# Performance work log

Hardware: AMD Instinct MI355X
Metric: run time of the kernel (lower is better)

The kernel has to match this reference:

```python
import jax, jax.numpy as jnp
import numpy as np

T = 4096
C = 2048
N_FEAT = 2048
NEG = -1e30  # finite stand-in for -inf so fully-masked (padding) rows stay NaN-free


def setup_inputs() -> dict:
    key = jax.random.key(0)
    kx, kw, kb = jax.random.split(key, 3)
    x = jax.random.normal(kx, (T, C), dtype=jnp.float32)
    # Dense(features=3*n_feat): kernel (C, 3*n_feat), bias (3*n_feat,)
    W = jax.random.normal(kw, (C, 3 * N_FEAT), dtype=jnp.float32) * (1.0 / np.sqrt(C))
    b = jax.random.normal(kb, (3 * N_FEAT,), dtype=jnp.float32) * 0.01
    n_padd = 128
    return {"x": x, "W": W, "b": b, "n_padd": n_padd}


def reference(x, W, b, n_padd):
    T_, _ = x.shape
    qkv = x @ W + b                      # (T, 3*n_feat)
    q, k, v = jnp.split(qkv, 3, axis=1)  # each (T, n_feat)
    scale = 1.0 / jnp.sqrt(jnp.float32(q.shape[1]))
    att = (q @ k.T) * scale              # (T, T)
    rows = jnp.arange(T_)[:, None]
    cols = jnp.arange(T_)[None, :]
    # causal AND both row/col past the left padding
    mask = (cols <= rows) & (cols >= n_padd) & (rows >= n_padd)
    att = jnp.where(mask, att, NEG)
    p = jax.nn.softmax(att, axis=1)      # stable row softmax
    # kernel only stores rows >= n_padd; padding rows are zero
    p = jnp.where(rows >= n_padd, p, 0.0)
    y = p @ v                            # (T, n_feat)
    return y
```

## Files before the change

### kernel.cpp

```cpp
#include <hip/hip_runtime.h>
#include <cstdint>


#define T_DIM 4096
#define C_DIM 2048
#define NF    2048
#define N3    6144
#define NEGV  (-1e30f)

typedef __bf16 bf16x8 __attribute__((ext_vector_type(8)));
typedef __bf16 bf16x4 __attribute__((ext_vector_type(4)));
typedef float  f32x4  __attribute__((ext_vector_type(4)));

#define FENCE() asm volatile("" ::: "memory")
#define BARRIER() do { FENCE(); __builtin_amdgcn_s_barrier(); FENCE(); } while (0)

__device__ __forceinline__ void async_cp16(const void* g, void* l) {
    __builtin_amdgcn_global_load_lds(
        reinterpret_cast<const __attribute__((address_space(1))) unsigned int*>(
            reinterpret_cast<uintptr_t>(g)),
        reinterpret_cast<__attribute__((address_space(3))) unsigned int*>(
            reinterpret_cast<uintptr_t>(l)),
        16, 0, 0);
}

__device__ __forceinline__ void gemm256(const __bf16* A, const __bf16* B,
                                        int lda, int ldb, int m0, int n0,
                                        int kiters, __bf16* As, __bf16* Bs,
                                        f32x4 (&acc)[8][4]) {
    if (kiters <= 0) return;
    const int t    = threadIdx.x;
    const int wv   = t >> 6;
    const int lane = t & 63;
    const int srow = t >> 3;
    const int scol = (((t & 7) ^ (srow & 7)) << 3);
    const int wmo  = (wv >> 2) * 128;
    const int wno  = (wv & 3) * 64;
    const int lrow = lane & 15;
    const int kq   = lane >> 4;
    const int swz  = lrow & 7;
    const int rc0  = ((kq ^ swz) << 3);
    const int rc1  = (((kq | 4) ^ swz) << 3);

    const __bf16* ga = A + (size_t)(m0 + srow) * lda + scol;
    const __bf16* gb = B + (size_t)(n0 + srow) * ldb + scol;

    auto stA4 = [&](int kk, int s) {
        const __bf16* a = ga + kk * 64;
#pragma unroll
        for (int j = 0; j < 4; ++j)
            async_cp16(a + (size_t)(64 * j) * lda,
                       &As[s * 16384 + j * 4096 + wv * 512]);
    };
    auto stB4 = [&](int kk, int s) {
        const __bf16* b2 = gb + kk * 64;
#pragma unroll
        for (int j = 0; j < 4; ++j)
            async_cp16(b2 + (size_t)(64 * j) * ldb,
                       &Bs[s * 16384 + j * 4096 + wv * 512]);
    };
    auto loadA4 = [&](const __bf16* Ab, int mh, int rc, bf16x8 (&af)[4]) {
#pragma unroll
        for (int mi = 0; mi < 4; ++mi)
            af[mi] = *(const bf16x8*)
                &Ab[(wmo + mh * 64 + mi * 16 + lrow) * 64 + rc];
    };
    auto loadB4 = [&](const __bf16* Bb, int rc, bf16x8 (&bfr)[4]) {
#pragma unroll
        for (int ni = 0; ni < 4; ++ni)
            bfr[ni] = *(const bf16x8*)&Bb[(wno + ni * 16 + lrow) * 64 + rc];
    };

    bf16x8 af[4], bfr[4];

    stA4(0, 0); stB4(0, 0);
    asm volatile("s_waitcnt vmcnt(0)" ::: "memory");
    BARRIER();

    for (int kt = 0; kt < kiters; ++kt) {
        const int b = kt & 1;
        const __bf16* Ab = &As[b * 16384];
        const __bf16* Bb = &Bs[b * 16384];
        const bool pf = (kt + 1 < kiters);

        loadB4(Bb, rc0, bfr);
        loadA4(Ab, 0, rc0, af);
        if (pf) stA4(kt + 1, b ^ 1);
        BARRIER();
        __builtin_amdgcn_s_setprio(1);
#pragma unroll
        for (int mi = 0; mi < 4; ++mi)
#pragma unroll
            for (int ni = 0; ni < 4; ++ni)
                acc[mi][ni] = __builtin_amdgcn_mfma_f32_16x16x32_bf16(
                    af[mi], bfr[ni], acc[mi][ni], 0, 0, 0);
        __builtin_amdgcn_s_setprio(0);
        BARRIER();
        loadA4(Ab, 1, rc0, af);
        if (pf) stB4(kt + 1, b ^ 1);
        BARRIER();
        __builtin_amdgcn_s_setprio(1);
#pragma unroll
        for (int mi = 0; mi < 4; ++mi)
#pragma unroll
            for (int ni = 0; ni < 4; ++ni)
                acc[4 + mi][ni] = __builtin_amdgcn_mfma_f32_16x16x32_bf16(
                    af[mi], bfr[ni], acc[4 + mi][ni], 0, 0, 0);
        __builtin_amdgcn_s_setprio(0);
        BARRIER();
        loadB4(Bb, rc1, bfr);
        loadA4(Ab, 0, rc1, af);
        BARRIER();
        __builtin_amdgcn_s_setprio(1);
#pragma unroll
        for (int mi = 0; mi < 4; ++mi)
#pragma unroll
            for (int ni = 0; ni < 4; ++ni)
                acc[mi][ni] = __builtin_amdgcn_mfma_f32_16x16x32_bf16(
                    af[mi], bfr[ni], acc[mi][ni], 0, 0, 0);
        __builtin_amdgcn_s_setprio(0);
        BARRIER();
        loadA4(Ab, 1, rc1, af);
        BARRIER();
        __builtin_amdgcn_s_setprio(1);
#pragma unroll
        for (int mi = 0; mi < 4; ++mi)
#pragma unroll
            for (int ni = 0; ni < 4; ++ni)
                acc[4 + mi][ni] = __builtin_amdgcn_mfma_f32_16x16x32_bf16(
                    af[mi], bfr[ni], acc[4 + mi][ni], 0, 0, 0);
        __builtin_amdgcn_s_setprio(0);
        if (pf) asm volatile("s_waitcnt vmcnt(0)" ::: "memory");
        BARRIER();
    }
}

#define EPI256()                                            \
    const int t = threadIdx.x, wv = t >> 6, lane = t & 63;  \
    const int wmo = (wv >> 2) * 128, wno = (wv & 3) * 64;   \
    const int rq = (lane >> 4) << 2, cn = lane & 15

__global__ void prep_kernel(const float* __restrict__ x,
                            __bf16* __restrict__ xb,
                            const float* __restrict__ W,
                            __bf16* __restrict__ Wt) {
    if (blockIdx.x < 2048) {
        const int n4 = (T_DIM * C_DIM) / 4;
        const int stride = 2048 * 256;
        for (int i = blockIdx.x * 256 + threadIdx.x; i < n4; i += stride) {
            float4 v = ((const float4*)x)[i];
            bf16x4 o;
            o[0] = (__bf16)v.x; o[1] = (__bf16)v.y;
            o[2] = (__bf16)v.z; o[3] = (__bf16)v.w;
            ((bf16x4*)xb)[i] = o;
        }
        return;
    }
    __shared__ float tile[32][33];
    const int tb = blockIdx.x - 2048;
    const int bx = (tb % (N3 / 32)) * 32;
    const int by = (tb / (N3 / 32)) * 32;
    const int tx = threadIdx.x & 31, ty = threadIdx.x >> 5;
#pragma unroll
    for (int i = 0; i < 32; i += 8)
        tile[ty + i][tx] = W[(size_t)(by + ty + i) * N3 + bx + tx];
    __syncthreads();
#pragma unroll
    for (int i = 0; i < 32; i += 8)
        Wt[(size_t)(bx + ty + i) * C_DIM + by + tx] = (__bf16)tile[tx][ty + i];
}

__global__ void __launch_bounds__(512)
qkv_gemm_kernel(const __bf16* __restrict__ xb, const __bf16* __restrict__ Wt,
                const float* __restrict__ bias, __bf16* __restrict__ qb,
                __bf16* __restrict__ kb, __bf16* __restrict__ vT) {
    __shared__ __bf16 As[2 * 256 * 64];
    __shared__ __bf16 Bs[2 * 256 * 64];
    f32x4 acc[8][4] = {};
    const int m0 = blockIdx.x * 256;
    const int by = blockIdx.y;
    const int n0 = by * 256;
    gemm256(xb, Wt, C_DIM, C_DIM, m0, n0, C_DIM / 64, As, Bs, acc);

    EPI256();
    if (by >= 16) {
#pragma unroll
        for (int mi = 0; mi < 8; ++mi)
#pragma unroll
            for (int ni = 0; ni < 4; ++ni) {
                int col = n0 + wno + ni * 16 + cn;
                float bv = bias[col];
                bf16x4 o;
#pragma unroll
                for (int r = 0; r < 4; ++r) o[r] = (__bf16)(acc[mi][ni][r] + bv);
                int row = m0 + wmo + mi * 16 + rq;
                *(bf16x4*)&vT[(size_t)(col - 2 * NF) * T_DIM + row] = o;
            }
    } else {
        __bf16* dst = (by < 8) ? qb : kb;
        const int coff = (by < 8) ? 0 : NF;
#pragma unroll
        for (int mi = 0; mi < 8; ++mi)
#pragma unroll
            for (int ni = 0; ni < 4; ++ni) {
                int col = n0 + wno + ni * 16 + cn;
                float bv = bias[col];
#pragma unroll
                for (int r = 0; r < 4; ++r) {
                    int row = m0 + wmo + mi * 16 + rq + r;
                    dst[(size_t)row * NF + (col - coff)] =
                        (__bf16)(acc[mi][ni][r] + bv);
                }
            }
    }
}

__global__ void __launch_bounds__(512)
sc_gemm_kernel(const __bf16* __restrict__ qb, const __bf16* __restrict__ kb,
               __bf16* __restrict__ S, const int* __restrict__ npadd_p) {
    int i = blockIdx.x;
    int mt = (int)((sqrtf(8.0f * (float)i + 1.0f) - 1.0f) * 0.5f);
    while ((mt + 1) * (mt + 2) / 2 <= i) ++mt;
    while (mt * (mt + 1) / 2 > i) --mt;
    int nt = i - mt * (mt + 1) / 2;
    const int m0 = mt * 256, n0 = nt * 256;
    const int npadd = *npadd_p;
    if (m0 + 256 <= npadd || n0 + 256 <= npadd) return;

    __shared__ __bf16 As[2 * 256 * 64];
    __shared__ __bf16 Bs[2 * 256 * 64];
    f32x4 acc[8][4] = {};
    gemm256(qb, kb, NF, NF, m0, n0, NF / 64, As, Bs, acc);

    const float scale = 0.022097086912079608f;
    EPI256();
#pragma unroll
    for (int mi = 0; mi < 8; ++mi)
#pragma unroll
        for (int ni = 0; ni < 4; ++ni) {
            int j = n0 + wno + ni * 16 + cn;
#pragma unroll
            for (int r = 0; r < 4; ++r) {
                int row = m0 + wmo + mi * 16 + rq + r;
                S[(size_t)row * T_DIM + j] = (__bf16)(acc[mi][ni][r] * scale);
            }
        }
}

__global__ void __launch_bounds__(256)
softmax_kernel(const __bf16* __restrict__ S, __bf16* __restrict__ P,
               const int* __restrict__ npadd_p) {
    const int wv = threadIdx.x >> 6, lane = threadIdx.x & 63;
    const int row = blockIdx.x * 4 + wv;
    const int npadd = *npadd_p;
    __bf16* prow = P + (size_t)row * T_DIM;

    if (row < npadd) {
        bf16x8 z = {};
#pragma unroll
        for (int c = 0; c < 8; ++c) ((bf16x8*)prow)[c * 64 + lane] = z;
        return;
    }

    const __bf16* srow = S + (size_t)row * T_DIM;
    float vals[64];
    float mx = NEGV;
#pragma unroll
    for (int c = 0; c < 8; ++c) {
        if (c * 512 > row) {
#pragma unroll
            for (int e = 0; e < 8; ++e) vals[c * 8 + e] = NEGV;
            continue;
        }
        int j0 = c * 512 + lane * 8;
        bf16x8 v = ((const bf16x8*)srow)[c * 64 + lane];
#pragma unroll
        for (int e = 0; e < 8; ++e) {
            float f = (j0 + e >= npadd && j0 + e <= row) ? (float)v[e] : NEGV;
            vals[c * 8 + e] = f;
            mx = fmaxf(mx, f);
        }
    }
#pragma unroll
    for (int o = 32; o > 0; o >>= 1) mx = fmaxf(mx, __shfl_xor(mx, o));

    float sm = 0.f;
#pragma unroll
    for (int k = 0; k < 64; ++k) {
        vals[k] = exp2f((vals[k] - mx) * 1.4426950408889634f);
        sm += vals[k];
    }
#pragma unroll
    for (int o = 32; o > 0; o >>= 1) sm += __shfl_xor(sm, o);
    float inv = 1.0f / sm;

#pragma unroll
    for (int c = 0; c < 8; ++c) {
        bf16x8 o;
#pragma unroll
        for (int e = 0; e < 8; ++e) o[e] = (__bf16)(vals[c * 8 + e] * inv);
        ((bf16x8*)prow)[c * 64 + lane] = o;
    }
}

__global__ void __launch_bounds__(512)
pv_gemm_kernel(const __bf16* __restrict__ P, const __bf16* __restrict__ vT,
               float* __restrict__ out, const int* __restrict__ npadd_p) {
    const int idx = blockIdx.x;
    const int kskip = *npadd_p >> 6;
    int mt, nt, start, iters;
    bool atomic_out;
    if (idx < 64) {
        mt = idx >> 3; nt = idx & 7;
        int ktt = (mt + 1) * 4 - kskip; if (ktt < 0) ktt = 0;
        start = kskip; iters = ktt; atomic_out = false;
    } else {
        int j = idx - 64;
        mt = 8 + ((j >> 3) & 7); nt = j & 7;
        int half = j >> 6;
        int ktt = (mt + 1) * 4 - kskip; if (ktt < 0) ktt = 0;
        int h0 = (ktt + 1) >> 1;
        start = kskip + (half ? h0 : 0);
        iters = half ? ktt - h0 : h0;
        atomic_out = true;
    }
    const int m0 = mt * 256, n0 = nt * 256;

    __shared__ __bf16 As[2 * 256 * 64];
    __shared__ __bf16 Bs[2 * 256 * 64];
    f32x4 acc[8][4] = {};
    gemm256(P + (size_t)start * 64, vT + (size_t)start * 64,
            T_DIM, T_DIM, m0, n0, iters, As, Bs, acc);

    EPI256();
#pragma unroll
    for (int mi = 0; mi < 8; ++mi)
#pragma unroll
        for (int ni = 0; ni < 4; ++ni) {
            int col = n0 + wno + ni * 16 + cn;
#pragma unroll
            for (int r = 0; r < 4; ++r) {
                int row = m0 + wmo + mi * 16 + rq + r;
                float* p = &out[(size_t)row * NF + col];
                if (atomic_out) unsafeAtomicAdd(p, acc[mi][ni][r]);
                else            *p = acc[mi][ni][r];
            }
        }
}

extern "C" void kernel_launch(void* const* d_in, const int* in_sizes, int n_in,
                              void* d_out, int out_size, void* d_ws,
                              size_t ws_size, hipStream_t stream) {
    const float* x = (const float*)d_in[0];
    const float* W = (const float*)d_in[1];
    const float* b = (const float*)d_in[2];
    const int* npadd = (const int*)d_in[3];
    float* out = (float*)d_out;

    char* ws = (char*)d_ws;
    __bf16* xb = (__bf16*)(ws);
    __bf16* Wt = (__bf16*)(ws + (16ull << 20));
    __bf16* qb = (__bf16*)(ws + (40ull << 20));
    __bf16* kb = (__bf16*)(ws + (56ull << 20));
    __bf16* vT = (__bf16*)(ws + (72ull << 20));
    __bf16* S  = (__bf16*)(ws + (88ull << 20));
    __bf16* P  = (__bf16*)(ws + (40ull << 20));

    hipMemsetAsync(out + (size_t)2048 * NF, 0, (size_t)2048 * NF * 4, stream);

    prep_kernel<<<2048 + (N3 / 32) * (C_DIM / 32), 256, 0, stream>>>(x, xb, W, Wt);
    qkv_gemm_kernel<<<dim3(T_DIM / 256, N3 / 256), 512, 0, stream>>>(xb, Wt, b,
                                                                     qb, kb, vT);
    sc_gemm_kernel<<<136, 512, 0, stream>>>(qb, kb, S, npadd);
    softmax_kernel<<<T_DIM / 4, 256, 0, stream>>>(S, P, npadd);
    pv_gemm_kernel<<<192, 512, 0, stream>>>(P, vT, out, npadd);
}
```

Baseline: 379.8 us.

## Triple-buffer A tiles in GEMM mainloop to prefetch two stages ahead

Result: slower. 394.6 us (+3.9%).

```diff
diff --git a/kernel.cpp b/kernel.cpp
--- a/kernel.cpp
+++ b/kernel.cpp
@@ -26,7 +26,7 @@
 
 __device__ __forceinline__ void gemm256(const __bf16* A, const __bf16* B,
                                         int lda, int ldb, int m0, int n0,
-                                        int kiters, __bf16* As, __bf16* Bs,
+                                        int kiters, __bf16* As3, __bf16* Bs2,
                                         f32x4 (&acc)[8][4]) {
     if (kiters <= 0) return;
     const int t    = threadIdx.x;
@@ -47,17 +47,17 @@
 
     auto stA4 = [&](int kk, int s) {
         const __bf16* a = ga + kk * 64;
+        __bf16* dst = As3 + s * 16384 + wv * 512;
 #pragma unroll
         for (int j = 0; j < 4; ++j)
-            async_cp16(a + (size_t)(64 * j) * lda,
-                       &As[s * 16384 + j * 4096 + wv * 512]);
+            async_cp16(a + (size_t)(64 * j) * lda, dst + j * 4096);
     };
     auto stB4 = [&](int kk, int s) {
         const __bf16* b2 = gb + kk * 64;
+        __bf16* dst = Bs2 + s * 16384 + wv * 512;
 #pragma unroll
         for (int j = 0; j < 4; ++j)
-            async_cp16(b2 + (size_t)(64 * j) * ldb,
-                       &Bs[s * 16384 + j * 4096 + wv * 512]);
+            async_cp16(b2 + (size_t)(64 * j) * ldb, dst + j * 4096);
     };
     auto loadA4 = [&](const __bf16* Ab, int mh, int rc, bf16x8 (&af)[4]) {
 #pragma unroll
@@ -73,19 +73,28 @@
 
     bf16x8 af[4], bfr[4];
 
-    stA4(0, 0); stB4(0, 0);
-    asm volatile("s_waitcnt vmcnt(0)" ::: "memory");
+    stB4(0, 0);
+    stA4(0, 0);
+    if (kiters > 1) {
+        stA4(1, 1);
+        asm volatile("s_waitcnt vmcnt(4)" ::: "memory");
+    } else {
+        asm volatile("s_waitcnt vmcnt(0)" ::: "memory");
+    }
     BARRIER();
 
+    int sa = 0, sb = 0;
     for (int kt = 0; kt < kiters; ++kt) {
-        const int b = kt & 1;
-        const __bf16* Ab = &As[b * 16384];
-        const __bf16* Bb = &Bs[b * 16384];
-        const bool pf = (kt + 1 < kiters);
-
+        const __bf16* Ab = As3 + sa * 16384;
+        const __bf16* Bb = Bs2 + sb * 16384;
+        const int sa2 = (sa >= 1) ? sa - 1 : sa + 2;
+        const bool pfB = (kt + 1 < kiters);
+        const bool pfA = (kt + 2 < kiters);
+
+        if (pfB) stB4(kt + 1, sb ^ 1);
+        if (pfA) stA4(kt + 2, sa2);
         loadB4(Bb, rc0, bfr);
         loadA4(Ab, 0, rc0, af);
-        if (pf) stA4(kt + 1, b ^ 1);
         BARRIER();
         __builtin_amdgcn_s_setprio(1);
 #pragma unroll
@@ -97,7 +106,6 @@
         __builtin_amdgcn_s_setprio(0);
         BARRIER();
         loadA4(Ab, 1, rc0, af);
-        if (pf) stB4(kt + 1, b ^ 1);
         BARRIER();
         __builtin_amdgcn_s_setprio(1);
 #pragma unroll
@@ -130,8 +138,12 @@
                 acc[4 + mi][ni] = __builtin_amdgcn_mfma_f32_16x16x32_bf16(
                     af[mi], bfr[ni], acc[4 + mi][ni], 0, 0, 0);
         __builtin_amdgcn_s_setprio(0);
-        if (pf) asm volatile("s_waitcnt vmcnt(0)" ::: "memory");
-        BARRIER();
+        if (pfA)       asm volatile("s_waitcnt vmcnt(4)" ::: "memory");
+        else if (pfB)  asm volatile("s_waitcnt vmcnt(0)" ::: "memory");
+        BARRIER();
+
+        sa = (sa == 2) ? 0 : sa + 1;
+        sb ^= 1;
     }
 }
 
@@ -174,13 +186,13 @@
 qkv_gemm_kernel(const __bf16* __restrict__ xb, const __bf16* __restrict__ Wt,
                 const float* __restrict__ bias, __bf16* __restrict__ qb,
                 __bf16* __restrict__ kb, __bf16* __restrict__ vT) {
-    __shared__ __bf16 As[2 * 256 * 64];
-    __shared__ __bf16 Bs[2 * 256 * 64];
+    __shared__ __bf16 As3[3 * 256 * 64];
+    __shared__ __bf16 Bs2[2 * 256 * 64];
     f32x4 acc[8][4] = {};
     const int m0 = blockIdx.x * 256;
     const int by = blockIdx.y;
     const int n0 = by * 256;
-    gemm256(xb, Wt, C_DIM, C_DIM, m0, n0, C_DIM / 64, As, Bs, acc);
+    gemm256(xb, Wt, C_DIM, C_DIM, m0, n0, C_DIM / 64, As3, Bs2, acc);
 
     EPI256();
     if (by >= 16) {
@@ -227,10 +239,10 @@
     const int npadd = *npadd_p;
     if (m0 + 256 <= npadd || n0 + 256 <= npadd) return;
 
-    __shared__ __bf16 As[2 * 256 * 64];
-    __shared__ __bf16 Bs[2 * 256 * 64];
+    __shared__ __bf16 As3[3 * 256 * 64];
+    __shared__ __bf16 Bs2[2 * 256 * 64];
     f32x4 acc[8][4] = {};
-    gemm256(qb, kb, NF, NF, m0, n0, NF / 64, As, Bs, acc);
+    gemm256(qb, kb, NF, NF, m0, n0, NF / 64, As3, Bs2, acc);
 
     const float scale = 0.022097086912079608f;
     EPI256();
@@ -326,11 +338,11 @@
     }
     const int m0 = mt * 256, n0 = nt * 256;
 
-    __shared__ __bf16 As[2 * 256 * 64];
-    __shared__ __bf16 Bs[2 * 256 * 64];
+    __shared__ __bf16 As3[3 * 256 * 64];
+    __shared__ __bf16 Bs2[2 * 256 * 64];
     f32x4 acc[8][4] = {};
     gemm256(P + (size_t)start * 64, vT + (size_t)start * 64,
-            T_DIM, T_DIM, m0, n0, iters, As, Bs, acc);
+            T_DIM, T_DIM, m0, n0, iters, As3, Bs2, acc);
 
     EPI256();
 #pragma unroll
```
